# Optimization experiments

Measured on AMD Instinct MI355X. Metric: run time of the kernel, lower is better.

The kernel has to match this reference:

```python
import jax, jax.numpy as jnp
import numpy as np

K = 512   # num_embeddings
D = 64    # embedding_dim
N = 262144

def l2norm(t, eps=1e-12):
    # matches F.normalize(t, p=2, dim=1)
    n = jnp.linalg.norm(t, axis=1, keepdims=True)
    return t / jnp.maximum(n, eps)

def setup_inputs() -> dict:
    key = jax.random.key(0)
    k1, k2, k3 = jax.random.split(key, 3)
    inputs = jax.random.normal(k1, (N, D), dtype=jnp.float32)
    labels = jax.random.randint(k2, (N,), 0, K)
    embedding = jax.random.normal(k3, (K, D), dtype=jnp.float32)  # frozen codebook (orthogonal init in original; random is fine for a numeric baseline)
    return {"inputs": inputs, "labels": labels, "embedding": embedding}

def reference(inputs, labels, embedding):
    # cosine distance path with labels != None
    flat = inputs.reshape(-1, D)
    distances = l2norm(flat) @ l2norm(embedding).T            # [N, K]
    encoding_indices = jnp.argmax(distances, axis=1)[:, None]  # [N, 1]
    encodings = jax.nn.one_hot(encoding_indices[:, 0], K, dtype=flat.dtype)  # [N, K] one-hot scatter
    quantized = (encodings @ embedding).reshape(inputs.shape)  # [N, D]
    # commitment loss: 1 - cosine sim at the supervised label index
    closs = (1.0 - jnp.take_along_axis(distances, labels[:, None], axis=1)[:, 0]).mean()
    loss = closs
    # straight-through estimator
    quantized = inputs + jax.lax.stop_gradient(quantized - inputs)
    perplexity = jnp.asarray(1, dtype=jnp.int32)
    return (loss, quantized, perplexity, encodings, encoding_indices)
```

## Files before the change

kernel.cpp:

```cpp
#include <hip/hip_runtime.h>
#include <hip/hip_bf16.h>

#define D_DIM 64
#define K_EMB 512
#define BM    128
#define XSTR  65
#define ESTR  68
#define RCAP  32768

typedef float f2v __attribute__((ext_vector_type(2)));

static constexpr size_t WS_RLIST = 16;
static constexpr size_t WS_ENT   = WS_RLIST + (size_t)RCAP * 4;
static constexpr size_t WS_EN64  = WS_ENT + (size_t)D_DIM * K_EMB * 4;

__global__ void prep_kernel(const float* __restrict__ emb,
                            float* __restrict__ entT,
                            double* __restrict__ en64,
                            double* __restrict__ loss_acc,
                            int* __restrict__ rcount) {
    const int k = blockIdx.x;
    const int d = threadIdx.x;
    double e = (double)emb[k * D_DIM + d];
    double sq = e * e;
    #pragma unroll
    for (int off = 32; off >= 1; off >>= 1) sq += __shfl_xor(sq, off);
    double inv = 1.0 / fmax(sqrt(sq), 1e-12);
    double v = e * inv;
    en64[(size_t)k * D_DIM + d] = v;
    entT[(size_t)d * K_EMB + k] = (float)v;
    if (k == 0 && d == 0) { *loss_acc = 0.0; *rcount = 0; }
}

__global__ __launch_bounds__(256, 2)
void main_kernel(const float* __restrict__ x, const int* __restrict__ labels,
                 const float* __restrict__ emb,
                 const float* __restrict__ entT, const double* __restrict__ en64,
                 double* __restrict__ loss_acc, int* __restrict__ rcount,
                 int* __restrict__ rlist,
                 float* __restrict__ out_quant, float* __restrict__ out_enc,
                 float* __restrict__ out_idx, int Ntot) {
    __shared__ float  Xs[BM][XSTR];
    __shared__ float  Es[D_DIM][ESTR];
    __shared__ float  xnrm[BM];
    __shared__ int    idxs[BM];
    __shared__ double lred[4];

    const int tid = threadIdx.x;
    const size_t row0 = (size_t)blockIdx.x * BM;

    #pragma unroll
    for (int i = 0; i < 8; ++i) {
        int f = tid + i * 256;
        int r = f >> 4;
        int d4 = (f & 15) << 2;
        float4 v = *reinterpret_cast<const float4*>(x + (row0 + r) * D_DIM + d4);
        Xs[r][d4 + 0] = v.x; Xs[r][d4 + 1] = v.y;
        Xs[r][d4 + 2] = v.z; Xs[r][d4 + 3] = v.w;
    }
    __syncthreads();

    {
        int r = tid >> 1, p = tid & 1;
        size_t row = row0 + r;
        int lab = labels[row];
        const double* el = en64 + (size_t)lab * D_DIM;
        double s2 = 0.0, dp = 0.0;
        #pragma unroll
        for (int j = 0; j < 32; ++j) {
            int d = p * 32 + j;
            double xv = (double)Xs[r][d];
            s2 = fma(xv, xv, s2);
            dp = fma(xv, el[d], dp);
        }
        s2 += __shfl_xor(s2, 1);
        dp += __shfl_xor(dp, 1);
        double contrib = 0.0;
        if (p == 0) {
            double nrm = sqrt(s2);
            xnrm[r] = (float)nrm;
            contrib = 1.0 - dp / fmax(nrm, 1e-12);
        }
        #pragma unroll
        for (int off = 32; off >= 1; off >>= 1) contrib += __shfl_xor(contrib, off);
        if ((tid & 63) == 0) lred[tid >> 6] = contrib;
    }
    __syncthreads();
    if (tid == 0) {
        double s = (lred[0] + lred[1]) + (lred[2] + lred[3]);
        atomicAdd(loss_acc, s / (double)Ntot);
    }

    const int kk0 = (tid & 7) * 8;
    const int r0  = (tid >> 3) * 4;

    float v1[4], v2[4];
    int   k1[4];
    #pragma unroll
    for (int i = 0; i < 4; ++i) { v1[i] = -1e30f; v2[i] = -1e30f; k1[i] = 0; }

    for (int c = 0; c < 8; ++c) {
        __syncthreads();
        #pragma unroll
        for (int i = 0; i < 4; ++i) {
            int f = tid + i * 256;
            int d = f >> 4;
            int k4 = (f & 15) << 2;
            float4 v = *reinterpret_cast<const float4*>(entT + (size_t)d * K_EMB + c * 64 + k4);
            *reinterpret_cast<float4*>(&Es[d][k4]) = v;
        }
        __syncthreads();

        float acc[4][8];
        #pragma unroll
        for (int i = 0; i < 4; ++i)
            #pragma unroll
            for (int j = 0; j < 8; ++j) acc[i][j] = 0.0f;

        #pragma unroll 4
        for (int d = 0; d < D_DIM; ++d) {
            float xv[4];
            #pragma unroll
            for (int i = 0; i < 4; ++i) xv[i] = Xs[r0 + i][d];
            float4 e0 = *reinterpret_cast<const float4*>(&Es[d][kk0]);
            float4 e1 = *reinterpret_cast<const float4*>(&Es[d][kk0 + 4]);
            float ev[8] = {e0.x, e0.y, e0.z, e0.w, e1.x, e1.y, e1.z, e1.w};
            #pragma unroll
            for (int i = 0; i < 4; ++i)
                #pragma unroll
                for (int j = 0; j < 8; ++j)
                    acc[i][j] = fmaf(xv[i], ev[j], acc[i][j]);
        }

        const int kbase = c * 64 + kk0;
        #pragma unroll
        for (int i = 0; i < 4; ++i) {
            #pragma unroll
            for (int j = 0; j < 8; ++j) {
                float v = acc[i][j];
                int kk = kbase + j;
                bool better = (v > v1[i]);
                v2[i] = better ? v1[i] : fmaxf(v2[i], v);
                k1[i] = better ? kk : k1[i];
                v1[i] = better ? v : v1[i];
            }
        }
    }

    #pragma unroll
    for (int off = 4; off >= 1; off >>= 1) {
        #pragma unroll
        for (int i = 0; i < 4; ++i) {
            float ov1 = __shfl_xor(v1[i], off);
            float ov2 = __shfl_xor(v2[i], off);
            int   ok1 = __shfl_xor(k1[i], off);
            bool takeB = (ov1 > v1[i]) || (ov1 == v1[i] && ok1 < k1[i]);
            float n2 = takeB ? fmaxf(v1[i], ov2) : fmaxf(ov1, v2[i]);
            v1[i] = takeB ? ov1 : v1[i];
            k1[i] = takeB ? ok1 : k1[i];
            v2[i] = n2;
        }
    }

    if ((tid & 7) == 0) {
        #pragma unroll
        for (int i = 0; i < 4; ++i) {
            int r = r0 + i;
            idxs[r] = k1[i];
            float margin = 1e-4f * xnrm[r] + 1e-7f;
            if (v1[i] - v2[i] < margin) {
                int slot = atomicAdd(rcount, 1);
                if (slot < RCAP) rlist[slot] = (int)(row0 + r);
            }
        }
    }
    __syncthreads();

    if (tid < BM) out_idx[row0 + tid] = (float)idxs[tid];

    #pragma unroll 4
    for (int i = 0; i < 32; ++i) {
        int f = tid + i * 256;
        int r = f >> 6;
        int d = f & 63;
        int kq = idxs[r];
        float q = emb[(size_t)kq * D_DIM + d];
        float xv = Xs[r][d];
        __builtin_nontemporal_store(xv + (q - xv), out_quant + (row0 + r) * D_DIM + d);
    }

    for (int i = 0; i < BM; ++i) {
        int kq = idxs[i];
        int k = tid * 2;
        f2v o;
        o.x = (k     == kq) ? 1.0f : 0.0f;
        o.y = (k + 1 == kq) ? 1.0f : 0.0f;
        __builtin_nontemporal_store(o, (f2v*)(out_enc + (row0 + i) * K_EMB + k));
    }
}

__global__ void refine_kernel(const float* __restrict__ x, const float* __restrict__ emb,
                              const double* __restrict__ en64,
                              const int* __restrict__ rcount, const int* __restrict__ rlist,
                              float* __restrict__ out_quant, float* __restrict__ out_enc,
                              float* __restrict__ out_idx) {
    int cnt = *rcount; if (cnt > RCAP) cnt = RCAP;
    const int lane = threadIdx.x & 63;
    const int wave = (blockIdx.x * blockDim.x + threadIdx.x) >> 6;
    const int nwaves = (gridDim.x * blockDim.x) >> 6;
    for (int s = wave; s < cnt; s += nwaves) {
        int row = rlist[s];
        const float* xr = x + (size_t)row * D_DIM;
        double best = -1e300; int bestk = 0;
        for (int j = 0; j < 8; ++j) {
            int k = j * 64 + lane;
            const double* e = en64 + (size_t)k * D_DIM;
            double acc = 0.0;
            #pragma unroll
            for (int d = 0; d < D_DIM; ++d)
                acc = fma((double)xr[d], e[d], acc);
            if (acc > best || (acc == best && k < bestk)) { best = acc; bestk = k; }
        }
        #pragma unroll
        for (int off = 32; off >= 1; off >>= 1) {
            double ov = __shfl_xor(best, off);
            int    ok = __shfl_xor(bestk, off);
            if (ov > best || (ov == best && ok < bestk)) { best = ov; bestk = ok; }
        }
        int old = (int)(out_idx[row] + 0.5f);
        if (bestk != old) {
            if (lane == 0) {
                out_idx[row] = (float)bestk;
                out_enc[(size_t)row * K_EMB + old]   = 0.0f;
                out_enc[(size_t)row * K_EMB + bestk] = 1.0f;
            }
            float q = emb[(size_t)bestk * D_DIM + lane];
            float xv = xr[lane];
            out_quant[(size_t)row * D_DIM + lane] = xv + (q - xv);
        }
    }
}

__global__ void final_kernel(const double* __restrict__ loss_acc,
                             float* __restrict__ out_loss,
                             float* __restrict__ out_perp) {
    if (threadIdx.x == 0) {
        out_loss[0] = (float)(*loss_acc);
        out_perp[0] = 1.0f;
    }
}

extern "C" void kernel_launch(void* const* d_in, const int* in_sizes, int n_in,
                              void* d_out, int out_size, void* d_ws, size_t ws_size,
                              hipStream_t stream) {
    const float* x      = (const float*)d_in[0];
    const int*   labels = (const int*)d_in[1];
    const float* emb    = (const float*)d_in[2];
    const int Ntot = in_sizes[0] / D_DIM;

    char* ws = (char*)d_ws;
    double* loss_acc = (double*)(ws);
    int*    rcount   = (int*)(ws + 8);
    int*    rlist    = (int*)(ws + WS_RLIST);
    float*  entT     = (float*)(ws + WS_ENT);
    double* en64     = (double*)(ws + WS_EN64);

    float* out       = (float*)d_out;
    float* out_loss  = out;
    float* out_quant = out + 1;
    float* out_perp  = out + 1 + (size_t)Ntot * D_DIM;
    float* out_enc   = out + 2 + (size_t)Ntot * D_DIM;
    float* out_idx   = out_enc + (size_t)Ntot * K_EMB;

    hipLaunchKernelGGL(prep_kernel, dim3(K_EMB), dim3(D_DIM), 0, stream,
                       emb, entT, en64, loss_acc, rcount);
    hipLaunchKernelGGL(main_kernel, dim3(Ntot / BM), dim3(256), 0, stream,
                       x, labels, emb, entT, en64, loss_acc, rcount, rlist,
                       out_quant, out_enc, out_idx, Ntot);
    hipLaunchKernelGGL(refine_kernel, dim3(128), dim3(256), 0, stream,
                       x, emb, en64, rcount, rlist, out_quant, out_enc, out_idx);
    hipLaunchKernelGGL(final_kernel, dim3(1), dim3(64), 0, stream,
                       loss_acc, out_loss, out_perp);
}
```

Before: 865.7 us.

## Transpose X tile in LDS and read codebook directly from global/L1

Stores the input tile transposed in shared memory so each thread can fetch its 4 rows with one float4 LDS read. It also drops the per-chunk staging of the codebook into shared memory and its two barriers, reading the normalized codebook straight from global memory through the cache instead. It raises the launch-bounds occupancy hint from 2 to 3 blocks, which the smaller LDS footprint allows. The risk is higher global/L1 load latency inside the inner FMA loop, and register pressure under the tighter bound.

```diff
diff --git a/kernel.cpp b/kernel.cpp
--- a/kernel.cpp
+++ b/kernel.cpp
@@ -4,8 +4,7 @@
 #define D_DIM 64
 #define K_EMB 512
 #define BM    128
-#define XSTR  65
-#define ESTR  68
+#define XTSTR 132
 #define RCAP  32768
 
 typedef float f2v __attribute__((ext_vector_type(2)));
@@ -32,7 +31,7 @@
     if (k == 0 && d == 0) { *loss_acc = 0.0; *rcount = 0; }
 }
 
-__global__ __launch_bounds__(256, 2)
+__global__ __launch_bounds__(256, 3)
 void main_kernel(const float* __restrict__ x, const int* __restrict__ labels,
                  const float* __restrict__ emb,
                  const float* __restrict__ entT, const double* __restrict__ en64,
@@ -40,8 +39,7 @@
                  int* __restrict__ rlist,
                  float* __restrict__ out_quant, float* __restrict__ out_enc,
                  float* __restrict__ out_idx, int Ntot) {
-    __shared__ float  Xs[BM][XSTR];
-    __shared__ float  Es[D_DIM][ESTR];
+    __shared__ float  XsT[D_DIM][XTSTR];
     __shared__ float  xnrm[BM];
     __shared__ int    idxs[BM];
     __shared__ double lred[4];
@@ -55,8 +53,8 @@
         int r = f >> 4;
         int d4 = (f & 15) << 2;
         float4 v = *reinterpret_cast<const float4*>(x + (row0 + r) * D_DIM + d4);
-        Xs[r][d4 + 0] = v.x; Xs[r][d4 + 1] = v.y;
-        Xs[r][d4 + 2] = v.z; Xs[r][d4 + 3] = v.w;
+        XsT[d4 + 0][r] = v.x; XsT[d4 + 1][r] = v.y;
+        XsT[d4 + 2][r] = v.z; XsT[d4 + 3][r] = v.w;
     }
     __syncthreads();
 
@@ -69,7 +67,7 @@
         #pragma unroll
         for (int j = 0; j < 32; ++j) {
             int d = p * 32 + j;
-            double xv = (double)Xs[r][d];
+            double xv = (double)XsT[d][r];
             s2 = fma(xv, xv, s2);
             dp = fma(xv, el[d], dp);
         }
@@ -100,16 +98,7 @@
     for (int i = 0; i < 4; ++i) { v1[i] = -1e30f; v2[i] = -1e30f; k1[i] = 0; }
 
     for (int c = 0; c < 8; ++c) {
-        __syncthreads();
-        #pragma unroll
-        for (int i = 0; i < 4; ++i) {
-            int f = tid + i * 256;
-            int d = f >> 4;
-            int k4 = (f & 15) << 2;
-            float4 v = *reinterpret_cast<const float4*>(entT + (size_t)d * K_EMB + c * 64 + k4);
-            *reinterpret_cast<float4*>(&Es[d][k4]) = v;
-        }
-        __syncthreads();
+        const float* eb = entT + c * 64 + kk0;
 
         float acc[4][8];
         #pragma unroll
@@ -119,17 +108,16 @@
 
         #pragma unroll 4
         for (int d = 0; d < D_DIM; ++d) {
-            float xv[4];
-            #pragma unroll
-            for (int i = 0; i < 4; ++i) xv[i] = Xs[r0 + i][d];
-            float4 e0 = *reinterpret_cast<const float4*>(&Es[d][kk0]);
-            float4 e1 = *reinterpret_cast<const float4*>(&Es[d][kk0 + 4]);
+            float4 xv = *reinterpret_cast<const float4*>(&XsT[d][r0]);
+            float4 e0 = *reinterpret_cast<const float4*>(eb + (size_t)d * K_EMB);
+            float4 e1 = *reinterpret_cast<const float4*>(eb + (size_t)d * K_EMB + 4);
+            float xr[4] = {xv.x, xv.y, xv.z, xv.w};
             float ev[8] = {e0.x, e0.y, e0.z, e0.w, e1.x, e1.y, e1.z, e1.w};
             #pragma unroll
             for (int i = 0; i < 4; ++i)
                 #pragma unroll
                 for (int j = 0; j < 8; ++j)
-                    acc[i][j] = fmaf(xv[i], ev[j], acc[i][j]);
+                    acc[i][j] = fmaf(xr[i], ev[j], acc[i][j]);
         }
 
         const int kbase = c * 64 + kk0;
@@ -185,7 +173,7 @@
         int d = f & 63;
         int kq = idxs[r];
         float q = emb[(size_t)kq * D_DIM + d];
-        float xv = Xs[r][d];
+        float xv = XsT[d][r];
         __builtin_nontemporal_store(xv + (q - xv), out_quant + (row0 + r) * D_DIM + d);
     }
 
```

Result: slower. 946.6 us (+9.3%).
